# Kernel optimization log

Measured on AMD Instinct MI355X. Metric: run time of the kernel, lower is better.

## Reference

```python
import jax, jax.numpy as jnp
import numpy as np

GRID_SIZE = 5
ORDER = 3  # spline_order
H_STEP = 2.0 / GRID_SIZE  # grid_range = [-1, 1]
GRID = jnp.arange(-ORDER, GRID_SIZE + ORDER + 1, dtype=jnp.float32) * H_STEP - 1.0  # (12,)


def b_splines(x):
    # x: (N, F) -> bases: (N, F, GRID_SIZE + ORDER) via Cox-de Boor recursion
    g = GRID
    xx = x[..., None]
    bases = ((xx >= g[:-1]) & (xx < g[1:])).astype(x.dtype)
    for k in range(1, ORDER + 1):
        left = (xx - g[:-(k + 1)]) / (g[k:-1] - g[:-(k + 1)]) * bases[..., :-1]
        right = (g[k + 1:] - xx) / (g[k + 1:] - g[1:-k]) * bases[..., 1:]
        bases = left + right
    return bases


def kan_linear(x, bw, sw, sc):
    # x: (N, F); bw: (O, F); sw: (O, F, C); sc: (O, F)
    base = jax.nn.silu(x) @ bw.T
    spline = jnp.einsum('nfc,ofc->no', b_splines(x), sw * sc[..., None])
    return base + spline


def kan_conv(x, bw, sw, sc):
    # x: (B, C, H, W); 3x3 patches, padding 1, stride 1 -> KANLinear over C*9 features
    B, C, H, W = x.shape
    patches = jax.lax.conv_general_dilated_patches(x, (3, 3), (1, 1), ((1, 1), (1, 1)))  # (B, C*9, H, W)
    p = patches.transpose(0, 2, 3, 1).reshape(B * H * W, C * 9)
    o = kan_linear(p, bw, sw, sc)  # (B*H*W, Cout)
    return o.reshape(B, H, W, -1).transpose(0, 3, 1, 2)


def maxpool2(x):
    B, C, H, W = x.shape
    return x.reshape(B, C, H // 2, 2, W // 2, 2).max(axis=(3, 5))


def setup_inputs() -> dict:
    key = jax.random.key(0)
    ks = jax.random.split(key, 32)
    d = {}
    d['x'] = jax.random.normal(ks[0], (128, 3, 32, 32), dtype=jnp.float32)
    conv_specs = [(3, 4), (4, 8), (8, 16), (16, 32)]
    i = 1
    for li, (cin, cout) in enumerate(conv_specs, 1):
        fin = cin * 9
        d[f'bw{li}'] = jax.random.normal(ks[i], (cout, fin), dtype=jnp.float32) * (1.0 / np.sqrt(fin)); i += 1
        d[f'sw{li}'] = jax.random.normal(ks[i], (cout, fin, GRID_SIZE + ORDER), dtype=jnp.float32) * 0.1; i += 1
        d[f'sc{li}'] = jax.random.normal(ks[i], (cout, fin), dtype=jnp.float32) * (1.0 / np.sqrt(fin)); i += 1
    lin_specs = [(2048, 2048), (1024, 2048), (10, 1024)]
    for li, (o, inn) in enumerate(lin_specs, 1):
        d[f'w{li}'] = jax.random.normal(ks[i], (o, inn), dtype=jnp.float32) * (1.0 / np.sqrt(inn)); i += 1
        d[f'b{li}'] = jnp.zeros((o,), dtype=jnp.float32); i += 1
    return d


def reference(x, bw1, sw1, sc1, bw2, sw2, sc2, bw3, sw3, sc3, bw4, sw4, sc4, w1, b1, w2, b2, w3, b3):
    x = kan_conv(x, bw1, sw1, sc1)
    x = kan_conv(x, bw2, sw2, sc2)
    x = maxpool2(x)
    x = kan_conv(x, bw3, sw3, sc3)
    x = kan_conv(x, bw4, sw4, sc4)
    x = maxpool2(x)
    x = x.reshape(x.shape[0], -1)  # (B, 32*8*8)
    x = jax.nn.relu(x @ w1.T + b1)
    x = jax.nn.relu(x @ w2.T + b2)
    return x @ w3.T + b3
```

## Files before the change

### kernel.cpp

```cpp
#include <hip/hip_runtime.h>

#define BATCH 128
#define AST 88

typedef __attribute__((ext_vector_type(8))) short bf16x8;
typedef __attribute__((ext_vector_type(16))) float f32x16;

__device__ __forceinline__ void spline_acts(float xv, float act[9]) {
    act[0] = xv * (1.0f / (1.0f + __expf(-xv)));
    float g[12];
#pragma unroll
    for (int i = 0; i < 12; ++i) g[i] = (float)(i - 3) * 0.4f - 1.0f;
    float bb[11];
#pragma unroll
    for (int c = 0; c < 11; ++c) bb[c] = (xv >= g[c] && xv < g[c + 1]) ? 1.0f : 0.0f;
#pragma unroll
    for (int k = 1; k <= 3; ++k) {
#pragma unroll
        for (int c = 0; c + k < 11; ++c) {
            float left  = (xv - g[c]) * (1.0f / (g[c + k] - g[c])) * bb[c];
            float right = (g[c + k + 1] - xv) * (1.0f / (g[c + k + 1] - g[c + 1])) * bb[c + 1];
            bb[c] = left + right;
        }
    }
#pragma unroll
    for (int c = 0; c < 8; ++c) act[c + 1] = bb[c];
}

__device__ __constant__ float ZPAD[9] = {0.0f, 0.0f, 0.0f, 0.02083333333f,
                                         0.47916666667f, 0.47916666667f,
                                         0.02083333333f, 0.0f, 0.0f};

__device__ __forceinline__ void bf16split(float x, ushort& h, ushort& l) {
    union { float f; unsigned u; } a; a.f = x;
    unsigned r = a.u + 0x7FFF + ((a.u >> 16) & 1);
    h = (ushort)(r >> 16);
    union { unsigned u; float f; } hf; hf.u = (unsigned)h << 16;
    union { float f; unsigned u; } bres; bres.f = x - hf.f;
    unsigned r2 = bres.u + 0x7FFF + ((bres.u >> 16) & 1);
    l = (ushort)(r2 >> 16);
}

__device__ __forceinline__ void pack_one(int i, const float* bw, const float* sw,
                                         const float* sc, float* out, int F, int O) {
    int o = i % O;
    int j = (i / O) % 9;
    int f = i / (9 * O);
    float v;
    if (j == 0) v = bw[o * F + f];
    else        v = sw[(o * F + f) * 8 + (j - 1)] * sc[o * F + f];
    out[i] = v;
}

__global__ void pack_all(const float* __restrict__ bw1, const float* __restrict__ sw1,
                         const float* __restrict__ sc1, const float* __restrict__ bw2,
                         const float* __restrict__ sw2, const float* __restrict__ sc2,
                         const float* __restrict__ bw3, const float* __restrict__ sw3,
                         const float* __restrict__ sc3, const float* __restrict__ bw4,
                         const float* __restrict__ sw4, const float* __restrict__ sc4,
                         float* __restrict__ ws) {
    int i = blockIdx.x * blockDim.x + threadIdx.x;
    if (i < 972)        pack_one(i,         bw1, sw1, sc1, ws,         27, 4);
    else if (i < 3564)  pack_one(i - 972,   bw2, sw2, sc2, ws + 972,   36, 8);
    else if (i < 13932) pack_one(i - 3564,  bw3, sw3, sc3, ws + 3564,  72, 16);
    else if (i < 55404) pack_one(i - 13932, bw4, sw4, sc4, ws + 13932, 144, 32);
}

__global__ void pack_frags(const float* __restrict__ wp1, const float* __restrict__ wp2,
                           const float* __restrict__ wp3, const float* __restrict__ wp4,
                           ushort* __restrict__ k1h, ushort* __restrict__ k1l,
                           ushort* __restrict__ k2h, ushort* __restrict__ k2l,
                           ushort* __restrict__ k3h, ushort* __restrict__ k3l,
                           ushort* __restrict__ k4h, ushort* __restrict__ k4l,
                           ushort* __restrict__ zph, ushort* __restrict__ zpl) {
    int i = blockIdx.x * 256 + threadIdx.x;
    if (i < 1152) {
        int l = i & 63, s = (i >> 6) & 1, t = i / 128;
#pragma unroll
        for (int e = 0; e < 8; ++e) {
            int k = s * 16 + ((l >> 5) * 8) + e, o = l & 31;
            float w = 0.f;
            if (k < 27 && o < 4) w = wp1[(((k / 9) * 9 + t) * 9 + (k % 9)) * 4 + o];
            ushort h, lo; bf16split(w, h, lo);
            k1h[i * 8 + e] = h; k1l[i * 8 + e] = lo;
        }
    } else if (i < 2880) {
        int q = i - 1152;
        int l = q & 63, s = (q >> 6) % 3, t = q / 192;
#pragma unroll
        for (int e = 0; e < 8; ++e) {
            int k = s * 16 + ((l >> 5) * 8) + e, o = l & 31;
            float w = 0.f;
            if (k < 36 && o < 8) w = wp2[(((k / 9) * 9 + t) * 9 + (k % 9)) * 8 + o];
            ushort h, lo; bf16split(w, h, lo);
            k2h[q * 8 + e] = h; k2l[q * 8 + e] = lo;
        }
    } else if (i < 5760) {
        int q = i - 2880;
        int l = q & 63, s = (q >> 6) % 5, t = q / 320;
#pragma unroll
        for (int e = 0; e < 8; ++e) {
            int k = s * 16 + ((l >> 5) * 8) + e, o = l & 31;
            float w = 0.f;
            if (k < 72 && o < 16) w = wp3[(((k / 9) * 9 + t) * 9 + (k % 9)) * 16 + o];
            ushort h, lo; bf16split(w, h, lo);
            k3h[q * 8 + e] = h; k3l[q * 8 + e] = lo;
        }
    } else if (i < 11520) {
        int q = i - 5760;
        int l = q & 63, s = (q >> 6) % 5, t = (q / 320) % 9, p = q / 2880;
#pragma unroll
        for (int e = 0; e < 8; ++e) {
            int k = s * 16 + ((l >> 5) * 8) + e, o = l & 31;
            float w = 0.f;
            if (k < 72) w = wp4[(((p * 8 + k / 9) * 9 + t) * 9 + (k % 9)) * 32 + o];
            ushort h, lo; bf16split(w, h, lo);
            k4h[q * 8 + e] = h; k4l[q * 8 + e] = lo;
        }
    } else if (i < 11600) {
        int c = i - 11520;
        ushort h, lo; bf16split(ZPAD[c % 9], h, lo);
        zph[c] = h; zpl[c] = lo;
    }
}

__global__ __launch_bounds__(256) void spline_x(const float* __restrict__ x,
                                                ushort* __restrict__ A1h,
                                                ushort* __restrict__ A1l) {
    __shared__ unsigned SB[7168];
    int i = blockIdx.x * 256 + threadIdx.x;
    int px = i & 1023, b = i >> 10;
    const float* xb = x + (size_t)b * 3072 + px;
    unsigned rh[14] = {}, rl[14] = {};
#pragma unroll
    for (int cin = 0; cin < 3; ++cin) {
        float a9[9];
        spline_acts(xb[cin * 1024], a9);
#pragma unroll
        for (int j = 0; j < 9; ++j) {
            ushort h, l2; bf16split(a9[j], h, l2);
            int c = cin * 9 + j;
            if (c & 1) { rh[c >> 1] |= (unsigned)h << 16; rl[c >> 1] |= (unsigned)l2 << 16; }
            else       { rh[c >> 1] |= h;                  rl[c >> 1] |= l2; }
        }
    }
    int wb = threadIdx.x * 14;
#pragma unroll
    for (int w = 0; w < 14; ++w) { SB[wb + w] = rh[w]; SB[3584 + wb + w] = rl[w]; }
    __syncthreads();
    const ushort* sb = (const ushort*)SB;
    size_t base = (size_t)blockIdx.x * 7168;
#pragma unroll
    for (int e = 0; e < 4; ++e) {
        int q = e * 256 + threadIdx.x;
        if (q < 896) {
            *(uint4*)(A1h + base + q * 8) = *(const uint4*)(sb + q * 8);
            *(uint4*)(A1l + base + q * 8) = *(const uint4*)(sb + 7168 + q * 8);
        }
    }
}

template <int KG, int CHG, int CHL, int ASTR, int KSTEPS, int NCO, int EPI>
__global__ __launch_bounds__(256) void conv_strip(
    const ushort* __restrict__ Agh, const ushort* __restrict__ Agl,
    const ushort* __restrict__ Bgh, const ushort* __restrict__ Bgl,
    const ushort* __restrict__ zph, const ushort* __restrict__ zpl,
    ushort* __restrict__ Oh, ushort* __restrict__ Ol) {
    __shared__ ushort AH[340 * ASTR];
    __shared__ ushort AL[340 * ASTR];
    const int tid = threadIdx.x;
    const int b = blockIdx.x >> 2, strip = blockIdx.x & 3;
    const int r0 = strip * 8;
    const int lane = tid & 63, wv = tid >> 6;

    {
        const ushort* ash = Agh + (size_t)b * 1024 * KG;
        const ushort* asl = Agl + (size_t)b * 1024 * KG;
        for (int idx = tid; idx < 320 * CHL; idx += 256) {
            int pxl = idx / CHL, ch = idx - pxl * CHL;
            int lr = pxl >> 5, c = pxl & 31;
            int grow = r0 - 1 + lr;
            uint2 vh, vl;
            if (ch >= CHG) { vh = make_uint2(0u, 0u); vl = make_uint2(0u, 0u); }
            else if ((unsigned)grow < 32u) {
                vh = *(const uint2*)(ash + (size_t)(grow * 32 + c) * KG + ch * 4);
                vl = *(const uint2*)(asl + (size_t)(grow * 32 + c) * KG + ch * 4);
            } else {
                vh = *(const uint2*)(zph + ch * 4);
                vl = *(const uint2*)(zpl + ch * 4);
            }
            int spx = lr * 34 + c + 1;
            *(uint2*)(&AH[spx * ASTR + ch * 4]) = vh;
            *(uint2*)(&AL[spx * ASTR + ch * 4]) = vl;
        }
        for (int idx = tid; idx < 20 * CHL; idx += 256) {
            int sel = idx / CHL, ch = idx - sel * CHL;
            int lr = sel >> 1, c = (sel & 1) ? 33 : 0;
            int spx = lr * 34 + c;
            uint2 vh, vl;
            if (ch >= CHG) { vh = make_uint2(0u, 0u); vl = make_uint2(0u, 0u); }
            else { vh = *(const uint2*)(zph + ch * 4); vl = *(const uint2*)(zpl + ch * 4); }
            *(uint2*)(&AH[spx * ASTR + ch * 4]) = vh;
            *(uint2*)(&AL[spx * ASTR + ch * 4]) = vl;
        }
    }
    __syncthreads();

    f32x16 acc0, acc1;
#pragma unroll
    for (int i = 0; i < 16; ++i) { acc0[i] = 0.f; acc1[i] = 0.f; }

    const int p0 = wv * 64 + (lane & 31);
    const int sp0 = ((p0 >> 5) + 1) * 34 + (p0 & 31) + 1;
    const int sp1 = sp0 + 34;
    const int koff = (lane >> 5) * 8;

#pragma unroll 1
    for (int t = 0; t < 9; ++t) {
        const int dA = ((t / 3) - 1) * 34 + (t % 3) - 1;
#pragma unroll
        for (int s = 0; s < KSTEPS; ++s) {
            bf16x8 a0h = *(const bf16x8*)(&AH[(sp0 + dA) * ASTR + s * 16 + koff]);
            bf16x8 a0l = *(const bf16x8*)(&AL[(sp0 + dA) * ASTR + s * 16 + koff]);
            bf16x8 a1h = *(const bf16x8*)(&AH[(sp1 + dA) * ASTR + s * 16 + koff]);
            bf16x8 a1l = *(const bf16x8*)(&AL[(sp1 + dA) * ASTR + s * 16 + koff]);
            bf16x8 bh = *(const bf16x8*)(Bgh + (size_t)((t * KSTEPS + s) * 64 + lane) * 8);
            bf16x8 bl = *(const bf16x8*)(Bgl + (size_t)((t * KSTEPS + s) * 64 + lane) * 8);
            acc0 = __builtin_amdgcn_mfma_f32_32x32x16_bf16(a0h, bh, acc0, 0, 0, 0);
            acc1 = __builtin_amdgcn_mfma_f32_32x32x16_bf16(a1h, bh, acc1, 0, 0, 0);
            acc0 = __builtin_amdgcn_mfma_f32_32x32x16_bf16(a0h, bl, acc0, 0, 0, 0);
            acc1 = __builtin_amdgcn_mfma_f32_32x32x16_bf16(a1h, bl, acc1, 0, 0, 0);
            acc0 = __builtin_amdgcn_mfma_f32_32x32x16_bf16(a0l, bh, acc0, 0, 0, 0);
            acc1 = __builtin_amdgcn_mfma_f32_32x32x16_bf16(a1l, bh, acc1, 0, 0, 0);
        }
    }
    __syncthreads();

    float* fl = (float*)AH;
    {
        int ccol = lane & 31;
        if (ccol < NCO) {
#pragma unroll
            for (int r = 0; r < 16; ++r) {
                int row = (r & 3) + 8 * (r >> 2) + 4 * (lane >> 5);
                fl[ccol * 257 + wv * 64 + row] = acc0[r];
                fl[ccol * 257 + wv * 64 + 32 + row] = acc1[r];
            }
        }
    }
    __syncthreads();

    if (EPI == 0) {
        unsigned* ubh = (unsigned*)AL;
        unsigned* ubl = (unsigned*)AH + 1032;
        unsigned rwh[18], rwl[18];
#pragma unroll
        for (int w = 0; w < 18; ++w) { rwh[w] = 0u; rwl[w] = 0u; }
#pragma unroll
        for (int co = 0; co < 4; ++co) {
            float a9[9];
            spline_acts(fl[co * 257 + tid], a9);
#pragma unroll
            for (int j = 0; j < 9; ++j) {
                ushort h, l2; bf16split(a9[j], h, l2);
                int c = co * 9 + j;
                if (c & 1) { rwh[c >> 1] |= (unsigned)h << 16; rwl[c >> 1] |= (unsigned)l2 << 16; }
                else       { rwh[c >> 1] |= h;                  rwl[c >> 1] |= l2; }
            }
        }
#pragma unroll
        for (int w = 0; w < 18; ++w) { ubh[tid * 18 + w] = rwh[w]; ubl[tid * 18 + w] = rwl[w]; }
        __syncthreads();
        size_t basew = ((size_t)b * 1024 + strip * 256) * 18;
        unsigned* goh = (unsigned*)Oh + basew;
        unsigned* gol = (unsigned*)Ol + basew;
#pragma unroll
        for (int e = 0; e < 18; ++e) {
            int q = e * 256 + tid;
            goh[q] = ubh[q];
            gol[q] = ubl[q];
        }
    } else {
        int cg = tid >> 6, pl = tid & 63;
        int phl = pl >> 4, pw = pl & 15;
        int base_m = (2 * phl) * 32 + 2 * pw;
        unsigned rwh[9], rwl[9];
#pragma unroll
        for (int w = 0; w < 9; ++w) { rwh[w] = 0u; rwl[w] = 0u; }
#pragma unroll
        for (int e = 0; e < 2; ++e) {
            int co = cg * 2 + e;
            const float* fb = fl + co * 257 + base_m;
            float m = fmaxf(fmaxf(fb[0], fb[1]), fmaxf(fb[32], fb[33]));
            float a9[9];
            spline_acts(m, a9);
#pragma unroll
            for (int j = 0; j < 9; ++j) {
                ushort h, l2; bf16split(a9[j], h, l2);
                int c = e * 9 + j;
                if (c & 1) { rwh[c >> 1] |= (unsigned)h << 16; rwl[c >> 1] |= (unsigned)l2 << 16; }
                else       { rwh[c >> 1] |= h;                  rwl[c >> 1] |= l2; }
            }
        }
        unsigned* ubh = (unsigned*)AL;
        unsigned* ubl = (unsigned*)AL + 2560;
#pragma unroll
        for (int w = 0; w < 9; ++w) {
            ubh[pl * 40 + cg * 9 + w] = rwh[w];
            ubl[pl * 40 + cg * 9 + w] = rwl[w];
        }
        if (cg == 3) {
#pragma unroll
            for (int w = 0; w < 4; ++w) { ubh[pl * 40 + 36 + w] = 0u; ubl[pl * 40 + 36 + w] = 0u; }
        }
        __syncthreads();
        size_t base = ((size_t)b * 256 + strip * 64) * 80;
        const ushort* sbh = (const ushort*)ubh;
        const ushort* sbl = (const ushort*)ubl;
#pragma unroll
        for (int e = 0; e < 3; ++e) {
            int q = e * 256 + tid;
            if (q < 640) {
                *(uint4*)(Oh + base + q * 8) = *(const uint4*)(sbh + q * 8);
                *(uint4*)(Ol + base + q * 8) = *(const uint4*)(sbl + q * 8);
            }
        }
    }
}

template <int NPH, int NCO, int POOL>
__global__ __launch_bounds__(256) void conv34(
    const ushort* __restrict__ Agh, const ushort* __restrict__ Agl,
    const ushort* __restrict__ Bgh, const ushort* __restrict__ Bgl,
    const ushort* __restrict__ zph, const ushort* __restrict__ zpl,
    ushort* __restrict__ Oh, ushort* __restrict__ Ol,
    float* __restrict__ pooled) {
    __shared__ ushort AH[180 * AST];
    __shared__ ushort AL[180 * AST];
    const int tid = threadIdx.x;
    const int b = blockIdx.x;
    const int half = blockIdx.y;
    const int r0 = half * 8;
    const int lane = tid & 63, wv = tid >> 6;

    f32x16 acc;
#pragma unroll
    for (int i = 0; i < 16; ++i) acc[i] = 0.f;

    const int m = wv * 32 + (lane & 31);
    const int spx = ((m >> 4) + 1) * 18 + (m & 15) + 1;
    const int koff = (lane >> 5) * 8;

#pragma unroll 1
    for (int p = 0; p < NPH; ++p) {
        if (p) __syncthreads();
        const ushort* ash = Agh + ((size_t)b * NPH + p) * 256 * 80;
        const ushort* asl = Agl + ((size_t)b * NPH + p) * 256 * 80;
#pragma unroll
        for (int e = 0; e < 8; ++e) {
            int idx = e * 256 + tid;
            if (idx < 1800) {
                int px = idx / 10, ch = idx - px * 10;
                int pr = px / 18, pc = px - pr * 18;
                int r = r0 - 1 + pr, c = pc - 1;
                bool inb = ((unsigned)r < 16u) && ((unsigned)c < 16u);
                uint4 vh, vl;
                if (inb) {
                    vh = *(const uint4*)(ash + (size_t)(r * 16 + c) * 80 + ch * 8);
                    vl = *(const uint4*)(asl + (size_t)(r * 16 + c) * 80 + ch * 8);
                } else {
                    vh = *(const uint4*)(zph + ch * 8);
                    vl = *(const uint4*)(zpl + ch * 8);
                }
                *(uint4*)(&AH[px * AST + ch * 8]) = vh;
                *(uint4*)(&AL[px * AST + ch * 8]) = vl;
            }
        }
        __syncthreads();

        const ushort* bsh = Bgh + (size_t)p * 2880 * 8;
        const ushort* bsl = Bgl + (size_t)p * 2880 * 8;
#pragma unroll 1
        for (int t = 0; t < 9; ++t) {
            const int dA = ((t / 3) - 1) * 18 + (t % 3) - 1;
#pragma unroll
            for (int s = 0; s < 5; ++s) {
                bf16x8 ah = *(const bf16x8*)(&AH[(spx + dA) * AST + s * 16 + koff]);
                bf16x8 al = *(const bf16x8*)(&AL[(spx + dA) * AST + s * 16 + koff]);
                bf16x8 bh = *(const bf16x8*)(bsh + (size_t)((t * 5 + s) * 64 + lane) * 8);
                bf16x8 bl = *(const bf16x8*)(bsl + (size_t)((t * 5 + s) * 64 + lane) * 8);
                acc = __builtin_amdgcn_mfma_f32_32x32x16_bf16(ah, bh, acc, 0, 0, 0);
                acc = __builtin_amdgcn_mfma_f32_32x32x16_bf16(ah, bl, acc, 0, 0, 0);
                acc = __builtin_amdgcn_mfma_f32_32x32x16_bf16(al, bh, acc, 0, 0, 0);
            }
        }
    }
    __syncthreads();

    float* fl = (float*)AH;
    {
        int ccol = lane & 31;
        if (ccol < NCO) {
#pragma unroll
            for (int r = 0; r < 16; ++r) {
                int row = (r & 3) + 8 * (r >> 2) + 4 * (lane >> 5);
                fl[ccol * 129 + wv * 32 + row] = acc[r];
            }
        }
    }
    __syncthreads();

    if (POOL == 1) {
#pragma unroll
        for (int e = 0; e < NCO * 32 / 256; ++e) {
            int idx = e * 256 + tid;
            int co = idx >> 5, pp = idx & 31;
            int prl = pp >> 3, pc = pp & 7;
            int mbase = (2 * prl) * 16 + 2 * pc;
            const float* fb = fl + co * 129 + mbase;
            float v = fmaxf(fmaxf(fb[0], fb[1]), fmaxf(fb[16], fb[17]));
            pooled[(size_t)b * 2048 + co * 64 + (r0 / 2 + prl) * 8 + pc] = v;
        }
    } else {
        unsigned* ubh = (unsigned*)AL;
        unsigned* ubl = (unsigned*)AH + 2064;
#pragma unroll 1
        for (int p2 = 0; p2 < 2; ++p2) {
            if (p2) __syncthreads();
            int px = tid & 127, cohalf = tid >> 7;
            unsigned rwh[18], rwl[18];
#pragma unroll
            for (int w = 0; w < 18; ++w) { rwh[w] = 0u; rwl[w] = 0u; }
#pragma unroll
            for (int e = 0; e < 4; ++e) {
                float v = fl[(p2 * 8 + cohalf * 4 + e) * 129 + px];
                float a9[9];
                spline_acts(v, a9);
#pragma unroll
                for (int j = 0; j < 9; ++j) {
                    ushort h, l2; bf16split(a9[j], h, l2);
                    int c = e * 9 + j;
                    if (c & 1) { rwh[c >> 1] |= (unsigned)h << 16; rwl[c >> 1] |= (unsigned)l2 << 16; }
                    else       { rwh[c >> 1] |= h;                  rwl[c >> 1] |= l2; }
                }
            }
            int wb = px * 40 + cohalf * 18;
#pragma unroll
            for (int w = 0; w < 18; ++w) { ubh[wb + w] = rwh[w]; ubl[wb + w] = rwl[w]; }
            if (cohalf) {
#pragma unroll
                for (int w = 0; w < 4; ++w) { ubh[px * 40 + 36 + w] = 0u; ubl[px * 40 + 36 + w] = 0u; }
            }
            __syncthreads();
            const ushort* sbh = (const ushort*)ubh;
            const ushort* sbl = (const ushort*)ubl;
            size_t base = ((size_t)(b * 2 + p2) * 256 + r0 * 16) * 80;
#pragma unroll
            for (int e = 0; e < 5; ++e) {
                int q = e * 256 + tid;
                if (q < 1280) {
                    *(uint4*)(Oh + base + q * 8) = *(const uint4*)(sbh + q * 8);
                    *(uint4*)(Ol + base + q * 8) = *(const uint4*)(sbl + q * 8);
                }
            }
        }
    }
}

template <int SPLIT>
__global__ __launch_bounds__(256) void fc_big(const float* __restrict__ A,
                                              const float* __restrict__ Wt,
                                              float* __restrict__ part,
                                              int M, int N, int K) {
    __shared__ float As[32][68];
    __shared__ float Ws[32][68];
    const int tid = threadIdx.x;
    const int tx = tid & 15, ty = tid >> 4;
    const int bm = blockIdx.y * 64, bn = blockIdx.x * 64;
    const int kc = K / SPLIT;
    const int kbeg = blockIdx.z * kc;
    float acc[4][4] = {};
    for (int k0 = kbeg; k0 < kbeg + kc; k0 += 32) {
#pragma unroll
        for (int e = 0; e < 8; ++e) {
            int g = e * 256 + tid;
            int k = g & 31, r = g >> 5;
            As[k][r] = A[(size_t)(bm + r) * K + k0 + k];
            Ws[k][r] = Wt[(size_t)(bn + r) * K + k0 + k];
        }
        __syncthreads();
#pragma unroll
        for (int kk = 0; kk < 32; ++kk) {
            float4 av = *(const float4*)(&As[kk][ty * 4]);
            float4 wv = *(const float4*)(&Ws[kk][tx * 4]);
            acc[0][0] = fmaf(av.x, wv.x, acc[0][0]);
            acc[0][1] = fmaf(av.x, wv.y, acc[0][1]);
            acc[0][2] = fmaf(av.x, wv.z, acc[0][2]);
            acc[0][3] = fmaf(av.x, wv.w, acc[0][3]);
            acc[1][0] = fmaf(av.y, wv.x, acc[1][0]);
            acc[1][1] = fmaf(av.y, wv.y, acc[1][1]);
            acc[1][2] = fmaf(av.y, wv.z, acc[1][2]);
            acc[1][3] = fmaf(av.y, wv.w, acc[1][3]);
            acc[2][0] = fmaf(av.z, wv.x, acc[2][0]);
            acc[2][1] = fmaf(av.z, wv.y, acc[2][1]);
            acc[2][2] = fmaf(av.z, wv.z, acc[2][2]);
            acc[2][3] = fmaf(av.z, wv.w, acc[2][3]);
            acc[3][0] = fmaf(av.w, wv.x, acc[3][0]);
            acc[3][1] = fmaf(av.w, wv.y, acc[3][1]);
            acc[3][2] = fmaf(av.w, wv.z, acc[3][2]);
            acc[3][3] = fmaf(av.w, wv.w, acc[3][3]);
        }
        __syncthreads();
    }
    float* p = part + (size_t)blockIdx.z * M * N;
#pragma unroll
    for (int i = 0; i < 4; ++i) {
        float4 v = make_float4(acc[i][0], acc[i][1], acc[i][2], acc[i][3]);
        *(float4*)&p[(size_t)(bm + ty * 4 + i) * N + (bn + tx * 4)] = v;
    }
}

template <int SPLIT>
__global__ void fc_reduce(const float* __restrict__ part, const float* __restrict__ bias,
                          float* __restrict__ C, int MN, int N, int relu) {
    int i = blockIdx.x * 256 + threadIdx.x;
    if (i >= MN) return;
    float s = bias[i % N];
#pragma unroll
    for (int z = 0; z < SPLIT; ++z) s += part[(size_t)z * MN + i];
    C[i] = relu ? fmaxf(s, 0.f) : s;
}

__global__ __launch_bounds__(256) void fc3_kernel(const float* __restrict__ A,
                                                  const float* __restrict__ Wt,
                                                  const float* __restrict__ bias,
                                                  float* __restrict__ C) {
    int gid = blockIdx.x * 256 + threadIdx.x;
    int wid = gid >> 6;
    int lane = gid & 63;
    int m = wid / 10, n = wid - m * 10;
    const float4* a = (const float4*)(A + (size_t)m * 1024);
    const float4* w = (const float4*)(Wt + (size_t)n * 1024);
    float s = 0.f;
#pragma unroll
    for (int it = 0; it < 4; ++it) {
        float4 av = a[it * 64 + lane];
        float4 wv = w[it * 64 + lane];
        s += av.x * wv.x + av.y * wv.y + av.z * wv.z + av.w * wv.w;
    }
#pragma unroll
    for (int off = 32; off; off >>= 1) s += __shfl_xor(s, off);
    if (lane == 0) C[wid] = s + bias[n];
}

extern "C" void kernel_launch(void* const* d_in, const int* in_sizes, int n_in,
                              void* d_out, int out_size, void* d_ws, size_t ws_size,
                              hipStream_t stream) {
    const float* x   = (const float*)d_in[0];
    const float* bw1 = (const float*)d_in[1];
    const float* sw1 = (const float*)d_in[2];
    const float* sc1 = (const float*)d_in[3];
    const float* bw2 = (const float*)d_in[4];
    const float* sw2 = (const float*)d_in[5];
    const float* sc2 = (const float*)d_in[6];
    const float* bw3 = (const float*)d_in[7];
    const float* sw3 = (const float*)d_in[8];
    const float* sc3 = (const float*)d_in[9];
    const float* bw4 = (const float*)d_in[10];
    const float* sw4 = (const float*)d_in[11];
    const float* sc4 = (const float*)d_in[12];
    const float* w1  = (const float*)d_in[13];
    const float* b1  = (const float*)d_in[14];
    const float* w2  = (const float*)d_in[15];
    const float* b2  = (const float*)d_in[16];
    const float* w3  = (const float*)d_in[17];
    const float* b3  = (const float*)d_in[18];

    float*  wsf = (float*)d_ws;
    ushort* wsu = (ushort*)d_ws;
    float* wp1 = wsf;
    float* wp2 = wsf + 972;
    float* wp3 = wsf + 3564;
    float* wp4 = wsf + 13932;
    ushort* k1h = wsu + 110848;
    ushort* k1l = wsu + 120064;
    ushort* k2h = wsu + 129280;
    ushort* k2l = wsu + 143104;
    ushort* k3h = wsu + 156928;
    ushort* k3l = wsu + 179968;
    ushort* k4h = wsu + 203008;
    ushort* k4l = wsu + 249088;
    ushort* zph = wsu + 295168;
    ushort* zpl = wsu + 295248;
    ushort* A1h = wsu + 524288;
    ushort* A1l = wsu + 4194304;
    ushort* A2h = wsu + 7864320;
    ushort* A2l = wsu + 12582912;
    ushort* A3h = wsu + 524288;
    ushort* A3l = wsu + 3145728;
    ushort* A4h = wsu + 5767168;
    ushort* A4l = wsu + 11010048;
    float* pooled = wsf + 262144;
    float* part1  = wsf + 524288;
    float* fc1o   = wsf + 2621440;
    float* part2  = wsf + 2883584;
    float* fc2o   = wsf + 3932160;

    pack_all<<<(55404 + 255) / 256, 256, 0, stream>>>(bw1, sw1, sc1, bw2, sw2, sc2,
                                                      bw3, sw3, sc3, bw4, sw4, sc4, wsf);
    pack_frags<<<46, 256, 0, stream>>>(wp1, wp2, wp3, wp4, k1h, k1l, k2h, k2l,
                                       k3h, k3l, k4h, k4l, zph, zpl);

    spline_x<<<512, 256, 0, stream>>>(x, A1h, A1l);
    conv_strip<28, 7, 8, 40, 2, 4, 0><<<512, 256, 0, stream>>>(A1h, A1l, k1h, k1l,
                                                               zph, zpl, A2h, A2l);
    conv_strip<36, 9, 12, 56, 3, 8, 1><<<512, 256, 0, stream>>>(A2h, A2l, k2h, k2l,
                                                                zph, zpl, A3h, A3l);
    conv34<1, 16, 0><<<dim3(128, 2), 256, 0, stream>>>(A3h, A3l, k3h, k3l, zph, zpl,
                                                       A4h, A4l, nullptr);
    conv34<2, 32, 1><<<dim3(128, 2), 256, 0, stream>>>(A4h, A4l, k4h, k4l, zph, zpl,
                                                       nullptr, nullptr, pooled);
    fc_big<8><<<dim3(32, 2, 8), 256, 0, stream>>>(pooled, w1, part1, 128, 2048, 2048);
    fc_reduce<8><<<1024, 256, 0, stream>>>(part1, b1, fc1o, 262144, 2048, 1);
    fc_big<8><<<dim3(16, 2, 8), 256, 0, stream>>>(fc1o, w2, part2, 128, 1024, 2048);
    fc_reduce<8><<<512, 256, 0, stream>>>(part2, b2, fc2o, 131072, 1024, 1);
    fc3_kernel<<<320, 256, 0, stream>>>(fc2o, w3, b3, (float*)d_out);
}
```

Measured before the change: 157.1 us.

## Split conv3/conv4 reduction across kernel rows and phases with separate reduce kernels

The conv34 kernels now split the 3x3 kernel-row and channel-phase reduction across extra grid blocks (z dimension). Each block writes fp32 partial sums to global memory, and new reduce kernels sum them and apply the spline activation packing or the max-pool. The aim is more parallelism on a GPU that the previous 256-block grid underfilled, and smaller LDS tiles per block. In exchange it adds global-memory traffic for the partials and two extra kernel launches.

```diff
diff --git a/kernel.cpp b/kernel.cpp
--- a/kernel.cpp
+++ b/kernel.cpp
@@ -328,41 +328,30 @@
     }
 }
 
-template <int NPH, int NCO, int POOL>
-__global__ __launch_bounds__(256) void conv34(
+template <int NPH, int NCO>
+__global__ __launch_bounds__(256) void conv34_part(
     const ushort* __restrict__ Agh, const ushort* __restrict__ Agl,
     const ushort* __restrict__ Bgh, const ushort* __restrict__ Bgl,
     const ushort* __restrict__ zph, const ushort* __restrict__ zpl,
-    ushort* __restrict__ Oh, ushort* __restrict__ Ol,
-    float* __restrict__ pooled) {
-    __shared__ ushort AH[180 * AST];
-    __shared__ ushort AL[180 * AST];
+    float* __restrict__ P) {
+    __shared__ ushort AH[144 * AST];
+    __shared__ ushort AL[144 * AST];
     const int tid = threadIdx.x;
-    const int b = blockIdx.x;
-    const int half = blockIdx.y;
+    const int b = blockIdx.x, half = blockIdx.y, z = blockIdx.z;
+    const int p = z / 3, g = z % 3;
     const int r0 = half * 8;
     const int lane = tid & 63, wv = tid >> 6;
 
-    f32x16 acc;
-#pragma unroll
-    for (int i = 0; i < 16; ++i) acc[i] = 0.f;
-
-    const int m = wv * 32 + (lane & 31);
-    const int spx = ((m >> 4) + 1) * 18 + (m & 15) + 1;
-    const int koff = (lane >> 5) * 8;
-
-#pragma unroll 1
-    for (int p = 0; p < NPH; ++p) {
-        if (p) __syncthreads();
+    {
         const ushort* ash = Agh + ((size_t)b * NPH + p) * 256 * 80;
         const ushort* asl = Agl + ((size_t)b * NPH + p) * 256 * 80;
 #pragma unroll
-        for (int e = 0; e < 8; ++e) {
+        for (int e = 0; e < 6; ++e) {
             int idx = e * 256 + tid;
-            if (idx < 1800) {
+            if (idx < 1440) {
                 int px = idx / 10, ch = idx - px * 10;
                 int pr = px / 18, pc = px - pr * 18;
-                int r = r0 - 1 + pr, c = pc - 1;
+                int r = r0 - 1 + g + pr, c = pc - 1;
                 bool inb = ((unsigned)r < 16u) && ((unsigned)c < 16u);
                 uint4 vh, vl;
                 if (inb) {
@@ -376,95 +365,106 @@
                 *(uint4*)(&AL[px * AST + ch * 8]) = vl;
             }
         }
-        __syncthreads();
-
-        const ushort* bsh = Bgh + (size_t)p * 2880 * 8;
-        const ushort* bsl = Bgl + (size_t)p * 2880 * 8;
-#pragma unroll 1
-        for (int t = 0; t < 9; ++t) {
-            const int dA = ((t / 3) - 1) * 18 + (t % 3) - 1;
-#pragma unroll
-            for (int s = 0; s < 5; ++s) {
-                bf16x8 ah = *(const bf16x8*)(&AH[(spx + dA) * AST + s * 16 + koff]);
-                bf16x8 al = *(const bf16x8*)(&AL[(spx + dA) * AST + s * 16 + koff]);
-                bf16x8 bh = *(const bf16x8*)(bsh + (size_t)((t * 5 + s) * 64 + lane) * 8);
-                bf16x8 bl = *(const bf16x8*)(bsl + (size_t)((t * 5 + s) * 64 + lane) * 8);
-                acc = __builtin_amdgcn_mfma_f32_32x32x16_bf16(ah, bh, acc, 0, 0, 0);
-                acc = __builtin_amdgcn_mfma_f32_32x32x16_bf16(ah, bl, acc, 0, 0, 0);
-                acc = __builtin_amdgcn_mfma_f32_32x32x16_bf16(al, bh, acc, 0, 0, 0);
-            }
-        }
     }
     __syncthreads();
 
-    float* fl = (float*)AH;
-    {
-        int ccol = lane & 31;
-        if (ccol < NCO) {
-#pragma unroll
-            for (int r = 0; r < 16; ++r) {
-                int row = (r & 3) + 8 * (r >> 2) + 4 * (lane >> 5);
-                fl[ccol * 129 + wv * 32 + row] = acc[r];
-            }
-        }
-    }
+    f32x16 acc;
+#pragma unroll
+    for (int i = 0; i < 16; ++i) acc[i] = 0.f;
+
+    const int m = wv * 32 + (lane & 31);
+    const int sbase = (m >> 4) * 18 + (m & 15);
+    const int koff = (lane >> 5) * 8;
+    const ushort* bsh = Bgh + (size_t)p * 2880 * 8;
+    const ushort* bsl = Bgl + (size_t)p * 2880 * 8;
+
+#pragma unroll
+    for (int dw = 0; dw < 3; ++dw) {
+        const int t = g * 3 + dw;
+#pragma unroll
+        for (int s = 0; s < 5; ++s) {
+            bf16x8 ah = *(const bf16x8*)(&AH[(sbase + dw) * AST + s * 16 + koff]);
+            bf16x8 al = *(const bf16x8*)(&AL[(sbase + dw) * AST + s * 16 + koff]);
+            bf16x8 bh = *(const bf16x8*)(bsh + (size_t)((t * 5 + s) * 64 + lane) * 8);
+            bf16x8 bl = *(const bf16x8*)(bsl + (size_t)((t * 5 + s) * 64 + lane) * 8);
+            acc = __builtin_amdgcn_mfma_f32_32x32x16_bf16(ah, bh, acc, 0, 0, 0);
+            acc = __builtin_amdgcn_mfma_f32_32x32x16_bf16(ah, bl, acc, 0, 0, 0);
+            acc = __builtin_amdgcn_mfma_f32_32x32x16_bf16(al, bh, acc, 0, 0, 0);
+        }
+    }
+
+    int co = lane & 31;
+    if (co < NCO) {
+        float* pb = P + ((size_t)(z * 256 + b * 2 + half) * 128) * NCO;
+#pragma unroll
+        for (int r = 0; r < 16; ++r) {
+            int px = wv * 32 + (r & 3) + 8 * (r >> 2) + 4 * (lane >> 5);
+            pb[px * NCO + co] = acc[r];
+        }
+    }
+}
+
+__global__ __launch_bounds__(256) void conv3_reduce(const float* __restrict__ P3,
+                                                    ushort* __restrict__ A4h,
+                                                    ushort* __restrict__ A4l) {
+    __shared__ unsigned UBH[10240], UBL[10240];
+    int b = blockIdx.x, p2 = blockIdx.y;
+    int px = threadIdx.x;
+    int bh = b * 2 + (px >> 7), lpx = px & 127;
+
+    unsigned rwh[40], rwl[40];
+#pragma unroll
+    for (int w = 0; w < 40; ++w) { rwh[w] = 0u; rwl[w] = 0u; }
+#pragma unroll
+    for (int e = 0; e < 8; ++e) {
+        int co = p2 * 8 + e;
+        float s = 0.f;
+#pragma unroll
+        for (int zz = 0; zz < 3; ++zz)
+            s += P3[((size_t)(zz * 256 + bh) * 128 + lpx) * 16 + co];
+        float a9[9];
+        spline_acts(s, a9);
+#pragma unroll
+        for (int j = 0; j < 9; ++j) {
+            ushort h, l2; bf16split(a9[j], h, l2);
+            int c = e * 9 + j;
+            if (c & 1) { rwh[c >> 1] |= (unsigned)h << 16; rwl[c >> 1] |= (unsigned)l2 << 16; }
+            else       { rwh[c >> 1] |= h;                  rwl[c >> 1] |= l2; }
+        }
+    }
+#pragma unroll
+    for (int w = 0; w < 40; ++w) { UBH[px * 40 + w] = rwh[w]; UBL[px * 40 + w] = rwl[w]; }
     __syncthreads();
-
-    if (POOL == 1) {
-#pragma unroll
-        for (int e = 0; e < NCO * 32 / 256; ++e) {
-            int idx = e * 256 + tid;
-            int co = idx >> 5, pp = idx & 31;
-            int prl = pp >> 3, pc = pp & 7;
-            int mbase = (2 * prl) * 16 + 2 * pc;
-            const float* fb = fl + co * 129 + mbase;
-            float v = fmaxf(fmaxf(fb[0], fb[1]), fmaxf(fb[16], fb[17]));
-            pooled[(size_t)b * 2048 + co * 64 + (r0 / 2 + prl) * 8 + pc] = v;
-        }
-    } else {
-        unsigned* ubh = (unsigned*)AL;
-        unsigned* ubl = (unsigned*)AH + 2064;
-#pragma unroll 1
-        for (int p2 = 0; p2 < 2; ++p2) {
-            if (p2) __syncthreads();
-            int px = tid & 127, cohalf = tid >> 7;
-            unsigned rwh[18], rwl[18];
-#pragma unroll
-            for (int w = 0; w < 18; ++w) { rwh[w] = 0u; rwl[w] = 0u; }
-#pragma unroll
-            for (int e = 0; e < 4; ++e) {
-                float v = fl[(p2 * 8 + cohalf * 4 + e) * 129 + px];
-                float a9[9];
-                spline_acts(v, a9);
-#pragma unroll
-                for (int j = 0; j < 9; ++j) {
-                    ushort h, l2; bf16split(a9[j], h, l2);
-                    int c = e * 9 + j;
-                    if (c & 1) { rwh[c >> 1] |= (unsigned)h << 16; rwl[c >> 1] |= (unsigned)l2 << 16; }
-                    else       { rwh[c >> 1] |= h;                  rwl[c >> 1] |= l2; }
-                }
-            }
-            int wb = px * 40 + cohalf * 18;
-#pragma unroll
-            for (int w = 0; w < 18; ++w) { ubh[wb + w] = rwh[w]; ubl[wb + w] = rwl[w]; }
-            if (cohalf) {
-#pragma unroll
-                for (int w = 0; w < 4; ++w) { ubh[px * 40 + 36 + w] = 0u; ubl[px * 40 + 36 + w] = 0u; }
-            }
-            __syncthreads();
-            const ushort* sbh = (const ushort*)ubh;
-            const ushort* sbl = (const ushort*)ubl;
-            size_t base = ((size_t)(b * 2 + p2) * 256 + r0 * 16) * 80;
-#pragma unroll
-            for (int e = 0; e < 5; ++e) {
-                int q = e * 256 + tid;
-                if (q < 1280) {
-                    *(uint4*)(Oh + base + q * 8) = *(const uint4*)(sbh + q * 8);
-                    *(uint4*)(Ol + base + q * 8) = *(const uint4*)(sbl + q * 8);
-                }
-            }
-        }
-    }
+    const ushort* sbh = (const ushort*)UBH;
+    const ushort* sbl = (const ushort*)UBL;
+    size_t base = ((size_t)(b * 2 + p2) * 256) * 80;
+#pragma unroll
+    for (int e = 0; e < 10; ++e) {
+        int q = e * 256 + px;
+        *(uint4*)(A4h + base + q * 8) = *(const uint4*)(sbh + q * 8);
+        *(uint4*)(A4l + base + q * 8) = *(const uint4*)(sbl + q * 8);
+    }
+}
+
+__global__ __launch_bounds__(256) void conv4_reduce_pool(const float* __restrict__ P4,
+                                                         float* __restrict__ pooled) {
+    int i = blockIdx.x * 256 + threadIdx.x;
+    int b = i >> 11, idx = i & 2047;
+    int co = idx >> 6, pp = idx & 63;
+    int pr = pp >> 3, pc = pp & 7;
+    int half = pr >> 2, lr = pr & 3;
+    int bh = b * 2 + half;
+    int px00 = (2 * lr) * 16 + 2 * pc;
+    float s00 = 0.f, s01 = 0.f, s10 = 0.f, s11 = 0.f;
+#pragma unroll
+    for (int zz = 0; zz < 6; ++zz) {
+        const float* pb = P4 + ((size_t)(zz * 256 + bh) * 128) * 32 + co;
+        s00 += pb[(size_t)px00 * 32];
+        s01 += pb[(size_t)(px00 + 1) * 32];
+        s10 += pb[(size_t)(px00 + 16) * 32];
+        s11 += pb[(size_t)(px00 + 17) * 32];
+    }
+    pooled[(size_t)b * 2048 + idx] = fmaxf(fmaxf(s00, s01), fmaxf(s10, s11));
 }
 
 template <int SPLIT>
@@ -600,6 +600,8 @@
     ushort* A3l = wsu + 3145728;
     ushort* A4h = wsu + 5767168;
     ushort* A4l = wsu + 11010048;
+    float* P3   = wsf + 9437184;
+    float* P4   = wsf + 11534336;
     float* pooled = wsf + 262144;
     float* part1  = wsf + 524288;
     float* fc1o   = wsf + 2621440;
@@ -616,10 +618,13 @@
                                                                zph, zpl, A2h, A2l);
     conv_strip<36, 9, 12, 56, 3, 8, 1><<<512, 256, 0, stream>>>(A2h, A2l, k2h, k2l,
                                                                 zph, zpl, A3h, A3l);
-    conv34<1, 16, 0><<<dim3(128, 2), 256, 0, stream>>>(A3h, A3l, k3h, k3l, zph, zpl,
-                                                       A4h, A4l, nullptr);
-    conv34<2, 32, 1><<<dim3(128, 2), 256, 0, stream>>>(A4h, A4l, k4h, k4l, zph, zpl,
-                                                       nullptr, nullptr, pooled);
+    conv34_part<1, 16><<<dim3(128, 2, 3), 256, 0, stream>>>(A3h, A3l, k3h, k3l,
+                                                            zph, zpl, P3);
+    conv3_reduce<<<dim3(128, 2), 256, 0, stream>>>(P3, A4h, A4l);
+    conv34_part<2, 32><<<dim3(128, 2, 6), 256, 0, stream>>>(A4h, A4l, k4h, k4l,
+                                                            zph, zpl, P4);
+    conv4_reduce_pool<<<1024, 256, 0, stream>>>(P4, pooled);
+
     fc_big<8><<<dim3(32, 2, 8), 256, 0, stream>>>(pooled, w1, part1, 128, 2048, 2048);
     fc_reduce<8><<<1024, 256, 0, stream>>>(part1, b1, fc1o, 262144, 2048, 1);
     fc_big<8><<<dim3(16, 2, 8), 256, 0, stream>>>(fc1o, w2, part2, 128, 1024, 2048);
```

Result: slower. 178.7 us (+13.8%).
